# Optimization experiments

Hardware: AMD Instinct MI355X
Metric: run time of the kernel (lower is better)

Reference implementation:

```python
import jax, jax.numpy as jnp
import numpy as np
from jax import lax

B, C, KH, SH, K = 128, 256, 7, 31, 3
EPS = 1e-5
DN = ('NCHW', 'OIHW', 'NCHW')


def _bn(x, p):
    # p: (4, C) rows = gamma, beta, running_mean, running_var (eval-mode BN)
    g, b, m, v = p[0], p[1], p[2], p[3]
    inv = g / jnp.sqrt(v + EPS)
    return x * inv[None, :, None, None] + (b - m * inv)[None, :, None, None]


def _dwconv(x, w):
    # depthwise 3x3 VALID conv, w: (C,1,K,K)
    return lax.conv_general_dilated(x, w, (1, 1), 'VALID', dimension_numbers=DN,
                                    feature_group_count=x.shape[1])


def _pwconv(x, w, b):
    y = lax.conv_general_dilated(x, w, (1, 1), 'VALID', dimension_numbers=DN)
    return y + b[None, :, None, None]


def _relu6(x):
    return jnp.minimum(jax.nn.relu(x), 6.0)


def _branch(x, dw_w, bn1, pw_w, pw_b, bn2):
    # Conv(dw,3x3,no bias) -> BN -> ReLU6 -> Conv(1x1) -> BN
    return _bn(_pwconv(_relu6(_bn(_dwconv(x, dw_w), bn1)), pw_w, pw_b), bn2)


def _xcorr_depthwise(search, kernel):
    # per-sample, per-channel cross-correlation via groups = B*C conv trick
    b, c, hs, ws = search.shape
    hk, wk = kernel.shape[2], kernel.shape[3]
    x = search.reshape(1, b * c, hs, ws)
    k = kernel.reshape(b * c, 1, hk, wk)
    out = lax.conv_general_dilated(x, k, (1, 1), 'VALID', dimension_numbers=DN,
                                   feature_group_count=b * c)
    return out.reshape(b, c, out.shape[2], out.shape[3])


def _bn_params(key):
    k1, k2, k3, k4 = jax.random.split(key, 4)
    g = jax.random.uniform(k1, (C,), minval=0.5, maxval=1.5)
    b = jax.random.normal(k2, (C,)) * 0.1
    m = jax.random.normal(k3, (C,)) * 0.1
    v = jax.random.uniform(k4, (C,), minval=0.5, maxval=1.5)
    return jnp.stack([g, b, m, v]).astype(jnp.float32)


def setup_inputs() -> dict:
    key = jax.random.key(0)
    ks = jax.random.split(key, 10)
    dw_std = np.float32(np.sqrt(2.0 / (K * K * C)))   # torch init: normal(0, sqrt(2/n))
    pw_std = np.float32(np.sqrt(2.0 / C))
    return {
        'kernel': jax.random.normal(ks[0], (B, C, KH, KH), jnp.float32),
        'search': jax.random.normal(ks[1], (B, C, SH, SH), jnp.float32),
        'k_dw_w': jax.random.normal(ks[2], (C, 1, K, K), jnp.float32) * dw_std,
        'k_bn1': _bn_params(ks[3]),
        'k_pw_w': jax.random.normal(ks[4], (C, C, 1, 1), jnp.float32) * pw_std,
        'k_pw_b': jnp.zeros((C,), jnp.float32),
        'k_bn2': _bn_params(ks[5]),
        's_dw_w': jax.random.normal(ks[6], (C, 1, K, K), jnp.float32) * dw_std,
        's_bn1': _bn_params(ks[7]),
        's_pw_w': jax.random.normal(ks[8], (C, C, 1, 1), jnp.float32) * pw_std,
        's_pw_b': jnp.zeros((C,), jnp.float32),
        's_bn2': _bn_params(ks[9]),
    }


def reference(kernel, search, k_dw_w, k_bn1, k_pw_w, k_pw_b, k_bn2,
              s_dw_w, s_bn1, s_pw_w, s_pw_b, s_bn2):
    k = _branch(kernel, k_dw_w, k_bn1, k_pw_w, k_pw_b, k_bn2)   # (B,C,5,5)
    s = _branch(search, s_dw_w, s_bn1, s_pw_w, s_pw_b, s_bn2)   # (B,C,29,29)
    return _xcorr_depthwise(s, k)                                # (B,C,25,25)
```

## Files before the change

### kernel.cpp

```cpp
#include <hip/hip_runtime.h>

constexpr int B = 128, C = 256;
constexpr float EPS = 1e-5f;
constexpr int NSG = B * 841;
constexpr int NKG = B * 25;

typedef unsigned short u16;
typedef short short8 __attribute__((ext_vector_type(8)));
typedef u16 u16x8 __attribute__((ext_vector_type(8)));
typedef float f32x4 __attribute__((ext_vector_type(4)));

__device__ __forceinline__ u16 bf16_rne(float x) {
    unsigned u = __builtin_bit_cast(unsigned, x);
    return (u16)((u + 0x7FFFu + ((u >> 16) & 1u)) >> 16);
}
__device__ __forceinline__ float bf16_f(u16 h) {
    return __builtin_bit_cast(float, (unsigned)h << 16);
}

#define GLOAD16(g, l)                                                              \
    __builtin_amdgcn_global_load_lds(                                              \
        (const __attribute__((address_space(1))) unsigned int*)(g),                \
        (__attribute__((address_space(3))) unsigned int*)(l), 16, 0, 0)

__global__ __launch_bounds__(256)
void wprep3(const float* __restrict__ ws, const float* __restrict__ wk,
            u16* __restrict__ WtS, u16* __restrict__ WtK) {
    int i = blockIdx.x * 256 + threadIdx.x;
    int co = i >> 8, k = i & 255;
    int t = k >> 5, cg = co >> 4;
    int lane = ((k >> 3) & 3) * 16 + (co & 15);
    int e = k & 7;
    size_t o = ((size_t)(t * 16 + cg) * 64 + lane) * 8 + e;
    WtS[o] = bf16_rne(ws[i]);
    WtK[o] = bf16_rne(wk[i]);
}

template<int IN_H, int CG, int NSLICE>
__global__ __launch_bounds__(256)
void dw_pass8(const float* __restrict__ in, const float* __restrict__ dw_w,
              const float* __restrict__ bn1, u16* __restrict__ X3) {
    constexpr int OUT_H = IN_H - 2, ON = OUT_H * OUT_H, IHW = IN_H * IN_H;
    constexpr int NSTRIP = (OUT_H + 7) / 8;
    constexpr int NF4 = CG * IHW / 4;
    constexpr int SUBS = CG / 8;
    constexpr int NSP = B * ON;
    constexpr int PADC = CG + 2;
    __shared__ __align__(16) float S[2][NF4 * 4 + 16];
    __shared__ __align__(16) u16 xt[ON * PADC];

    const int tid = threadIdx.x;
    const int b = blockIdx.x;
    const int g0 = blockIdx.y * NSLICE;

    const bool active = tid < CG * OUT_H;
    int cl = 0, oh = 0;
    if (active) { cl = tid / OUT_H; oh = tid - cl * OUT_H; }

    auto issue_stage = [&](int buf, int g) {
        const float* src = in + ((size_t)b * C + g * CG) * IHW;
        #pragma unroll
        for (int ii = 0; ii < (NF4 + 255) / 256; ++ii) {
            int q = ii * 256 + tid;
            if (q < NF4) GLOAD16(src + q * 4, (char*)S[buf] + q * 16);
        }
    };

    issue_stage(0, g0);
    int cur = 0;

    for (int it = 0; it < NSLICE; ++it) {
        const int g = g0 + it;
        const int ci0 = g * CG;
        asm volatile("s_waitcnt vmcnt(0)" ::: "memory");
        __syncthreads();

        if (it + 1 < NSLICE) issue_stage(cur ^ 1, g0 + it + 1);

        u16 outv[NSTRIP][8];
        if (active) {
            const int ci = ci0 + cl;
            float wreg[9];
            #pragma unroll
            for (int q = 0; q < 9; ++q) wreg[q] = dw_w[ci * 9 + q];
            const float inv = bn1[ci] * rsqrtf(bn1[3 * C + ci] + EPS);
            const float shv = bn1[C + ci] - bn1[2 * C + ci] * inv;
            #pragma unroll
            for (int s = 0; s < NSTRIP; ++s) {
                float res[8] = {0.f, 0.f, 0.f, 0.f, 0.f, 0.f, 0.f, 0.f};
                #pragma unroll
                for (int dy = 0; dy < 3; ++dy) {
                    const float* r = S[cur] + cl * IHW + (oh + dy) * IN_H + s * 8;
                    float x[10];
                    #pragma unroll
                    for (int j = 0; j < 10; ++j) x[j] = r[j];
                    #pragma unroll
                    for (int o = 0; o < 8; ++o)
                        res[o] = fmaf(x[o], wreg[dy * 3],
                                  fmaf(x[o + 1], wreg[dy * 3 + 1],
                                   fmaf(x[o + 2], wreg[dy * 3 + 2], res[o])));
                }
                #pragma unroll
                for (int o = 0; o < 8; ++o) {
                    float y = res[o] * inv + shv;
                    y = fminf(fmaxf(y, 0.f), 6.f);
                    outv[s][o] = bf16_rne(y);
                }
            }
        }
        __syncthreads();

        if (active) {
            #pragma unroll
            for (int s = 0; s < NSTRIP; ++s) {
                const int ow0 = s * 8;
                #pragma unroll
                for (int o = 0; o < 8; ++o) {
                    if (ow0 + o < OUT_H) {
                        int n = oh * OUT_H + ow0 + o;
                        xt[n * PADC + cl] = outv[s][o];
                    }
                }
            }
        }
        __syncthreads();

        for (int q = tid; q < ON * SUBS; q += 256) {
            int sub = q / ON, n = q - sub * ON;
            const unsigned* w = (const unsigned*)xt + n * (PADC / 2) + sub * 4;
            uint4 v = {w[0], w[1], w[2], w[3]};
            u16* dst = X3 + ((size_t)(g * SUBS + sub) * NSP + (size_t)b * ON + n) * 8;
            *(uint4*)dst = v;
        }
        cur ^= 1;
    }
}

template<int IN_H, int CG>
__global__ __launch_bounds__(256)
void dw_pass7(const float* __restrict__ in, const float* __restrict__ dw_w,
              const float* __restrict__ bn1, u16* __restrict__ X3) {
    constexpr int OUT_H = IN_H - 2, ON = OUT_H * OUT_H, IHW = IN_H * IN_H;
    constexpr int NSTRIP = (OUT_H + 7) / 8;
    constexpr int NFLT = CG * IHW;
    constexpr int NF4 = NFLT / 4;
    constexpr int SUBS = CG / 8;
    constexpr int NSP = B * ON;
    constexpr int PADC = CG + 2;
    constexpr unsigned SM_IN = (NFLT + 16) * 4;
    constexpr unsigned SM_XT = (unsigned)ON * PADC * 2;
    constexpr unsigned SMSZ = SM_IN > SM_XT ? SM_IN : SM_XT;
    __shared__ __align__(16) char SMEM[SMSZ];
    float* S = (float*)SMEM;
    u16* xt = (u16*)SMEM;

    const int tid = threadIdx.x;
    const int b = blockIdx.x, g = blockIdx.y;
    const int ci0 = g * CG;
    const float* src = in + ((size_t)b * C + ci0) * IHW;

    for (int q = tid; q < NF4; q += 256)
        ((float4*)S)[q] = ((const float4*)src)[q];
    __syncthreads();

    const bool active = tid < CG * OUT_H;
    int cl = 0, oh = 0;
    if (active) { cl = tid / OUT_H; oh = tid - cl * OUT_H; }
    u16 outv[NSTRIP][8];
    if (active) {
        const int ci = ci0 + cl;
        float wreg[9];
        #pragma unroll
        for (int q = 0; q < 9; ++q) wreg[q] = dw_w[ci * 9 + q];
        const float inv = bn1[ci] * rsqrtf(bn1[3 * C + ci] + EPS);
        const float shv = bn1[C + ci] - bn1[2 * C + ci] * inv;
        #pragma unroll
        for (int s = 0; s < NSTRIP; ++s) {
            float res[8] = {0.f, 0.f, 0.f, 0.f, 0.f, 0.f, 0.f, 0.f};
            #pragma unroll
            for (int dy = 0; dy < 3; ++dy) {
                const float* r = S + cl * IHW + (oh + dy) * IN_H + s * 8;
                float x[10];
                #pragma unroll
                for (int j = 0; j < 10; ++j) x[j] = r[j];
                #pragma unroll
                for (int o = 0; o < 8; ++o)
                    res[o] = fmaf(x[o], wreg[dy * 3],
                              fmaf(x[o + 1], wreg[dy * 3 + 1],
                               fmaf(x[o + 2], wreg[dy * 3 + 2], res[o])));
            }
            #pragma unroll
            for (int o = 0; o < 8; ++o) {
                float y = res[o] * inv + shv;
                y = fminf(fmaxf(y, 0.f), 6.f);
                outv[s][o] = bf16_rne(y);
            }
        }
    }
    __syncthreads();

    if (active) {
        #pragma unroll
        for (int s = 0; s < NSTRIP; ++s) {
            const int ow0 = s * 8;
            #pragma unroll
            for (int o = 0; o < 8; ++o) {
                if (ow0 + o < OUT_H) {
                    int n = oh * OUT_H + ow0 + o;
                    xt[n * PADC + cl] = outv[s][o];
                }
            }
        }
    }
    __syncthreads();

    for (int q = tid; q < ON * SUBS; q += 256) {
        int sub = q / ON, n = q - sub * ON;
        const unsigned* w = (const unsigned*)xt + n * (PADC / 2) + sub * 4;
        uint4 v = {w[0], w[1], w[2], w[3]};
        u16* dst = X3 + ((size_t)(g * SUBS + sub) * NSP + (size_t)b * ON + n) * 8;
        *(uint4*)dst = v;
    }
}

template<int PQ>
__global__ __launch_bounds__(256)
void gemm7(const u16* __restrict__ X3, const u16* __restrict__ Wt,
           const float* __restrict__ pw_b, const float* __restrict__ bn2,
           u16* __restrict__ out) {
    constexpr int NSP = B * PQ;
    const int lane = threadIdx.x & 63, wave = threadIdx.x >> 6;
    const int lh = lane >> 4, ll = lane & 15;
    const int n0 = blockIdx.x * 64;

    f32x4 acc[4][4] = {};
    short8 bx0[4], aw0[4], bx1[4], aw1[4];

#define LOADX(t, bx)                                                            \
    {                                                                           \
        _Pragma("unroll")                                                       \
        for (int j = 0; j < 4; ++j) {                                           \
            size_t off = ((size_t)((t) * 4 + lh) * NSP + n0 + j * 16 + ll) * 8; \
            bx[j] = *(const short8*)(X3 + off);                                 \
        }                                                                       \
    }
#define LOADW(t, aw)                                                            \
    {                                                                           \
        _Pragma("unroll")                                                       \
        for (int i = 0; i < 4; ++i) {                                           \
            size_t off = ((size_t)((t) * 16 + wave * 4 + i) * 64 + lane) * 8;   \
            aw[i] = *(const short8*)(Wt + off);                                 \
        }                                                                       \
    }
#define MM(aw, bx)                                                              \
    {                                                                           \
        _Pragma("unroll")                                                       \
        for (int i = 0; i < 4; ++i) {                                           \
            _Pragma("unroll")                                                   \
            for (int j = 0; j < 4; ++j)                                         \
                acc[i][j] = __builtin_amdgcn_mfma_f32_16x16x32_bf16(aw[i], bx[j], acc[i][j], 0, 0, 0); \
        }                                                                       \
    }

    LOADX(0, bx0); LOADW(0, aw0);
    #pragma unroll
    for (int tt = 0; tt < 8; tt += 2) {
        if (tt + 1 < 8) { LOADX(tt + 1, bx1); LOADW(tt + 1, aw1); }
        MM(aw0, bx0);
        if (tt + 2 < 8) { LOADX(tt + 2, bx0); LOADW(tt + 2, aw0); }
        if (tt + 1 < 8) { MM(aw1, bx1); }
    }
#undef LOADX
#undef LOADW
#undef MM

    int bj[4], pj[4];
    #pragma unroll
    for (int j = 0; j < 4; ++j) {
        int nn = n0 + j * 16 + ll;
        bj[j] = nn / PQ; pj[j] = nn - bj[j] * PQ;
    }
    #pragma unroll
    for (int i = 0; i < 4; ++i) {
        #pragma unroll
        for (int r = 0; r < 4; ++r) {
            int co = wave * 64 + i * 16 + lh * 4 + r;
            float inv = bn2[co] * rsqrtf(bn2[3 * C + co] + EPS);
            float sh  = bn2[C + co] - bn2[2 * C + co] * inv + pw_b[co] * inv;
            #pragma unroll
            for (int j = 0; j < 4; ++j)
                out[((size_t)bj[j] * C + co) * PQ + pj[j]] = bf16_rne(acc[i][j][r] * inv + sh);
        }
    }
}

__global__ __launch_bounds__(256)
void xcorr3(const u16* __restrict__ s, const u16* __restrict__ k,
            float* __restrict__ out) {
    const int bc0 = blockIdx.x * 10;
    const int nbc = min(10, B * C - bc0);
    __shared__ float ss[10 * 841];
    __shared__ float ks[10 * 25];
    const int tid = threadIdx.x;
    for (int i = tid; i < nbc * 841; i += 256) ss[i] = bf16_f(s[(size_t)bc0 * 841 + i]);
    for (int i = tid; i < nbc * 25; i += 256) ks[i] = bf16_f(k[(size_t)bc0 * 25 + i]);
    __syncthreads();

    const int lb = tid / 25, lt = tid - lb * 25;
    if (lb >= nbc) return;
    const int ohg = lt / 5, owg = lt - ohg * 5;
    const float* sp = ss + lb * 841 + (ohg * 5) * 29 + owg * 5;
    float kk[25];
    #pragma unroll
    for (int q = 0; q < 25; ++q) kk[q] = ks[lb * 25 + q];

    float acc[5][5] = {};
    #pragma unroll
    for (int ir = 0; ir < 9; ++ir) {
        float row[9];
        #pragma unroll
        for (int j = 0; j < 9; ++j) row[j] = sp[ir * 29 + j];
        #pragma unroll
        for (int oi = 0; oi < 5; ++oi) {
            int ki = ir - oi;
            if (ki < 0 || ki > 4) continue;
            #pragma unroll
            for (int oj = 0; oj < 5; ++oj)
                #pragma unroll
                for (int kj = 0; kj < 5; ++kj)
                    acc[oi][oj] = fmaf(row[oj + kj], kk[ki * 5 + kj], acc[oi][oj]);
        }
    }
    float* op = out + (size_t)(bc0 + lb) * 625;
    #pragma unroll
    for (int oi = 0; oi < 5; ++oi)
        #pragma unroll
        for (int oj = 0; oj < 5; ++oj)
            op[(ohg * 5 + oi) * 25 + owg * 5 + oj] = acc[oi][oj];
}

template<int IN_H>
__global__ __launch_bounds__(256)
void branch_fallback(const float* __restrict__ in, const float* __restrict__ dw_w,
                     const float* __restrict__ bn1, const float* __restrict__ pw_w,
                     const float* __restrict__ pw_b, const float* __restrict__ bn2,
                     float* __restrict__ out) {
    constexpr int OUT_H = IN_H - 2;
    constexpr int P = OUT_H * OUT_H;
    const int n0  = blockIdx.x * 64;
    const int co0 = blockIdx.y * 64;
    const int tid = threadIdx.x;
    const int tx = tid & 15, ty = tid >> 4;
    __shared__ __align__(16) float Ws[16][64];
    __shared__ __align__(16) float Xs2[16][64];
    float acc[4][4] = {};
    for (int k0 = 0; k0 < C; k0 += 16) {
        #pragma unroll
        for (int e = 0; e < 4; e++) {
            int idx = e * 256 + tid;
            int m = idx & 63, kk = idx >> 6;
            Ws[kk][m] = pw_w[(co0 + m) * C + (k0 + kk)];
        }
        #pragma unroll
        for (int e = 0; e < 4; e++) {
            int idx = e * 256 + tid;
            int nn = idx & 63, kk = idx >> 6;
            int ci = k0 + kk;
            int n = n0 + nn;
            int b = n / P, p = n - b * P;
            int oh = p / OUT_H, ow = p - oh * OUT_H;
            const float* ip = in + (((size_t)b * C + ci) * IN_H + oh) * IN_H + ow;
            const float* wp = dw_w + ci * 9;
            float s = 0.f;
            #pragma unroll
            for (int dy = 0; dy < 3; dy++)
                #pragma unroll
                for (int dx = 0; dx < 3; dx++)
                    s = fmaf(ip[dy * IN_H + dx], wp[dy * 3 + dx], s);
            float inv = bn1[ci] * rsqrtf(bn1[3 * C + ci] + EPS);
            float y = s * inv + (bn1[C + ci] - bn1[2 * C + ci] * inv);
            Xs2[kk][nn] = fminf(fmaxf(y, 0.f), 6.f);
        }
        __syncthreads();
        #pragma unroll
        for (int kk = 0; kk < 16; kk++) {
            float4 av = *reinterpret_cast<const float4*>(&Ws[kk][ty * 4]);
            float4 bv = *reinterpret_cast<const float4*>(&Xs2[kk][tx * 4]);
            float a[4] = {av.x, av.y, av.z, av.w};
            float bb[4] = {bv.x, bv.y, bv.z, bv.w};
            #pragma unroll
            for (int i = 0; i < 4; i++)
                #pragma unroll
                for (int j = 0; j < 4; j++)
                    acc[i][j] = fmaf(a[i], bb[j], acc[i][j]);
        }
        __syncthreads();
    }
    #pragma unroll
    for (int i = 0; i < 4; i++) {
        int co = co0 + ty * 4 + i;
        float inv = bn2[co] * rsqrtf(bn2[3 * C + co] + EPS);
        float sh  = (bn2[C + co] - bn2[2 * C + co] * inv) + pw_b[co] * inv;
        int n = n0 + tx * 4;
        #pragma unroll
        for (int j = 0; j < 4; j++) {
            int nj = n + j;
            int bj2 = nj / P, pj2 = nj - bj2 * P;
            out[((size_t)bj2 * C + co) * P + pj2] = acc[i][j] * inv + sh;
        }
    }
}

__global__ __launch_bounds__(256)
void xcorr2f(const float* __restrict__ s, const float* __restrict__ k,
             float* __restrict__ out) {
    const int bc0 = blockIdx.x * 10;
    const int nbc = min(10, B * C - bc0);
    __shared__ float ss[10 * 841];
    __shared__ float ks[10 * 25];
    const int tid = threadIdx.x;
    for (int i = tid; i < nbc * 841; i += 256) ss[i] = s[(size_t)bc0 * 841 + i];
    for (int i = tid; i < nbc * 25; i += 256) ks[i] = k[(size_t)bc0 * 25 + i];
    __syncthreads();
    const int lb = tid / 25, lt = tid - lb * 25;
    if (lb >= nbc) return;
    const int ohg = lt / 5, owg = lt - ohg * 5;
    const float* sp = ss + lb * 841 + (ohg * 5) * 29 + owg * 5;
    float kk[25];
    #pragma unroll
    for (int q = 0; q < 25; ++q) kk[q] = ks[lb * 25 + q];
    float acc[5][5] = {};
    #pragma unroll
    for (int ir = 0; ir < 9; ++ir) {
        float row[9];
        #pragma unroll
        for (int j = 0; j < 9; ++j) row[j] = sp[ir * 29 + j];
        #pragma unroll
        for (int oi = 0; oi < 5; ++oi) {
            int ki = ir - oi;
            if (ki < 0 || ki > 4) continue;
            #pragma unroll
            for (int oj = 0; oj < 5; ++oj)
                #pragma unroll
                for (int kj = 0; kj < 5; ++kj)
                    acc[oi][oj] = fmaf(row[oj + kj], kk[ki * 5 + kj], acc[oi][oj]);
        }
    }
    float* op = out + (size_t)(bc0 + lb) * 625;
    #pragma unroll
    for (int oi = 0; oi < 5; ++oi)
        #pragma unroll
        for (int oj = 0; oj < 5; ++oj)
            op[(ohg * 5 + oi) * 25 + owg * 5 + oj] = acc[oi][oj];
}

extern "C" void kernel_launch(void* const* d_in, const int* in_sizes, int n_in,
                              void* d_out, int out_size, void* d_ws, size_t ws_size,
                              hipStream_t stream) {
    const float* kernel = (const float*)d_in[0];
    const float* search = (const float*)d_in[1];
    const float* k_dw_w = (const float*)d_in[2];
    const float* k_bn1  = (const float*)d_in[3];
    const float* k_pw_w = (const float*)d_in[4];
    const float* k_pw_b = (const float*)d_in[5];
    const float* k_bn2  = (const float*)d_in[6];
    const float* s_dw_w = (const float*)d_in[7];
    const float* s_bn1  = (const float*)d_in[8];
    const float* s_pw_w = (const float*)d_in[9];
    const float* s_pw_b = (const float*)d_in[10];
    const float* s_bn2  = (const float*)d_in[11];

    constexpr size_t SB_B  = (size_t)NSG * C * 2;
    constexpr size_t KB_B  = (size_t)NKG * C * 2;
    constexpr size_t X3S_B = (size_t)NSG * C * 2;
    constexpr size_t X3K_B = (size_t)NKG * C * 2;
    constexpr size_t W_B   = (size_t)C * C * 2;
    constexpr size_t NEED  = SB_B + KB_B + X3S_B + X3K_B + 2 * W_B;

    if (ws_size >= NEED) {
        char* base = (char*)d_ws;
        u16* Sb   = (u16*)base;   base += SB_B;
        u16* Kb   = (u16*)base;   base += KB_B;
        u16* X3s  = (u16*)base;   base += X3S_B;
        u16* X3k  = (u16*)base;   base += X3K_B;
        u16* WtS  = (u16*)base;   base += W_B;
        u16* WtK  = (u16*)base;

        wprep3<<<dim3(256), dim3(256), 0, stream>>>(s_pw_w, k_pw_w, WtS, WtK);
        dw_pass8<31, 8, 4><<<dim3(B, 8), dim3(256), 0, stream>>>(search, s_dw_w, s_bn1, X3s);
        dw_pass7<7, 32><<<dim3(B, 8), dim3(256), 0, stream>>>(kernel, k_dw_w, k_bn1, X3k);
        gemm7<841><<<dim3(NSG / 64), dim3(256), 0, stream>>>(X3s, WtS, s_pw_b, s_bn2, Sb);
        gemm7<25><<<dim3(NKG / 64), dim3(256), 0, stream>>>(X3k, WtK, k_pw_b, k_bn2, Kb);
        xcorr3<<<dim3((B * C + 9) / 10), dim3(256), 0, stream>>>(Sb, Kb, (float*)d_out);
    } else {
        float* s_buf = (float*)d_ws;
        float* k_buf = s_buf + (size_t)B * C * 29 * 29;
        branch_fallback<7><<<dim3(50, 4), dim3(256), 0, stream>>>(
            kernel, k_dw_w, k_bn1, k_pw_w, k_pw_b, k_bn2, k_buf);
        branch_fallback<31><<<dim3(1682, 4), dim3(256), 0, stream>>>(
            search, s_dw_w, s_bn1, s_pw_w, s_pw_b, s_bn2, s_buf);
        xcorr2f<<<dim3((B * C + 9) / 10), dim3(256), 0, stream>>>(s_buf, k_buf, (float*)d_out);
    }
}
```

Measured before the change: 142.6 us.

## Make search depthwise pass wave-local with per-wave LDS and no block barriers

The search-branch depthwise kernel changes from a 256-thread block that double-buffers four 8-channel slices with several __syncthreads per slice to 128-thread blocks in which each wave owns one 8-channel group. Each wave stages its group into a private LDS segment, computes the conv, BN and ReLU6 into registers, then reuses the same LDS as the transpose buffer, ordered only by waitcnt and scheduling barriers. The grid doubles and the intra-block pipelining goes away. This removes block-wide barrier stalls and raises the number of independent blocks, at the cost of no load/compute overlap within a wave and more registers per lane, since each lane handles several row tasks.

Result: slower. 155.3 us (+9.0%).

```diff
diff --git a/kernel.cpp b/kernel.cpp
--- a/kernel.cpp
+++ b/kernel.cpp
@@ -36,103 +36,109 @@
     WtK[o] = bf16_rne(wk[i]);
 }
 
-template<int IN_H, int CG, int NSLICE>
-__global__ __launch_bounds__(256)
-void dw_pass8(const float* __restrict__ in, const float* __restrict__ dw_w,
+template<int IN_H, int CG, int WPB>
+__global__ __launch_bounds__(WPB * 64)
+void dw_pass9(const float* __restrict__ in, const float* __restrict__ dw_w,
               const float* __restrict__ bn1, u16* __restrict__ X3) {
     constexpr int OUT_H = IN_H - 2, ON = OUT_H * OUT_H, IHW = IN_H * IN_H;
     constexpr int NSTRIP = (OUT_H + 7) / 8;
     constexpr int NF4 = CG * IHW / 4;
-    constexpr int SUBS = CG / 8;
     constexpr int NSP = B * ON;
     constexpr int PADC = CG + 2;
-    __shared__ __align__(16) float S[2][NF4 * 4 + 16];
-    __shared__ __align__(16) u16 xt[ON * PADC];
-
-    const int tid = threadIdx.x;
-    const int b = blockIdx.x;
-    const int g0 = blockIdx.y * NSLICE;
-
-    const bool active = tid < CG * OUT_H;
-    int cl = 0, oh = 0;
-    if (active) { cl = tid / OUT_H; oh = tid - cl * OUT_H; }
-
-    auto issue_stage = [&](int buf, int g) {
-        const float* src = in + ((size_t)b * C + g * CG) * IHW;
-        #pragma unroll
-        for (int ii = 0; ii < (NF4 + 255) / 256; ++ii) {
-            int q = ii * 256 + tid;
-            if (q < NF4) GLOAD16(src + q * 4, (char*)S[buf] + q * 16);
-        }
-    };
-
-    issue_stage(0, g0);
-    int cur = 0;
-
-    for (int it = 0; it < NSLICE; ++it) {
-        const int g = g0 + it;
-        const int ci0 = g * CG;
-        asm volatile("s_waitcnt vmcnt(0)" ::: "memory");
-        __syncthreads();
-
-        if (it + 1 < NSLICE) issue_stage(cur ^ 1, g0 + it + 1);
-
-        u16 outv[NSTRIP][8];
-        if (active) {
-            const int ci = ci0 + cl;
-            float wreg[9];
-            #pragma unroll
-            for (int q = 0; q < 9; ++q) wreg[q] = dw_w[ci * 9 + q];
-            const float inv = bn1[ci] * rsqrtf(bn1[3 * C + ci] + EPS);
-            const float shv = bn1[C + ci] - bn1[2 * C + ci] * inv;
-            #pragma unroll
-            for (int s = 0; s < NSTRIP; ++s) {
-                float res[8] = {0.f, 0.f, 0.f, 0.f, 0.f, 0.f, 0.f, 0.f};
-                #pragma unroll
-                for (int dy = 0; dy < 3; ++dy) {
-                    const float* r = S[cur] + cl * IHW + (oh + dy) * IN_H + s * 8;
-                    float x[10];
-                    #pragma unroll
-                    for (int j = 0; j < 10; ++j) x[j] = r[j];
-                    #pragma unroll
-                    for (int o = 0; o < 8; ++o)
-                        res[o] = fmaf(x[o], wreg[dy * 3],
-                                  fmaf(x[o + 1], wreg[dy * 3 + 1],
-                                   fmaf(x[o + 2], wreg[dy * 3 + 2], res[o])));
-                }
-                #pragma unroll
-                for (int o = 0; o < 8; ++o) {
-                    float y = res[o] * inv + shv;
-                    y = fminf(fmaxf(y, 0.f), 6.f);
-                    outv[s][o] = bf16_rne(y);
-                }
+    constexpr int RT = (CG * OUT_H + 63) / 64;
+    constexpr int SEG = ((NF4 * 16 + 63) / 64) * 64;
+    __shared__ __align__(16) char SMEM[WPB][SEG];
+
+    const int lane = threadIdx.x & 63, w = threadIdx.x >> 6;
+    const int b = blockIdx.x, g = blockIdx.y;
+    const int kc  = g * WPB + w;
+    const int ci0 = kc * CG;
+    char* S8 = SMEM[w];
+    const float* src = in + ((size_t)b * C + ci0) * IHW;
+
+    #pragma unroll
+    for (int r = 0; r < (NF4 + 63) / 64; ++r) {
+        int q = r * 64 + lane;
+        if (q < NF4) GLOAD16(src + q * 4, S8 + q * 16);
+    }
+    asm volatile("s_waitcnt vmcnt(0)" ::: "memory");
+    __builtin_amdgcn_sched_barrier(0);
+
+    const float* S = (const float*)S8;
+    u16* xt = (u16*)S8;
+
+    u16x8 ov[RT * NSTRIP];
+    bool actv[RT];
+    int clv[RT], ohv[RT];
+    #pragma unroll
+    for (int r = 0; r < RT; ++r) {
+        const int task = r * 64 + lane;
+        const bool act = task < CG * OUT_H;
+        actv[r] = act;
+        const int cl = act ? task / OUT_H : 0;
+        const int oh = act ? task - cl * OUT_H : 0;
+        clv[r] = cl; ohv[r] = oh;
+        const int ci = ci0 + cl;
+        float wreg[9];
+        #pragma unroll
+        for (int q = 0; q < 9; ++q) wreg[q] = dw_w[ci * 9 + q];
+        const float inv = bn1[ci] * rsqrtf(bn1[3 * C + ci] + EPS);
+        const float shv = bn1[C + ci] - bn1[2 * C + ci] * inv;
+        #pragma unroll
+        for (int s = 0; s < NSTRIP; ++s) {
+            float res[8] = {0.f, 0.f, 0.f, 0.f, 0.f, 0.f, 0.f, 0.f};
+            #pragma unroll
+            for (int dy = 0; dy < 3; ++dy) {
+                const float* rp = S + cl * IHW + (oh + dy) * IN_H + s * 8;
+                float x[10];
+                #pragma unroll
+                for (int j = 0; j < 10; ++j) x[j] = rp[j];
+                #pragma unroll
+                for (int o = 0; o < 8; ++o)
+                    res[o] = fmaf(x[o], wreg[dy * 3],
+                              fmaf(x[o + 1], wreg[dy * 3 + 1],
+                               fmaf(x[o + 2], wreg[dy * 3 + 2], res[o])));
             }
-        }
-        __syncthreads();
-
-        if (active) {
+            u16x8 pv;
+            #pragma unroll
+            for (int o = 0; o < 8; ++o) {
+                float y = res[o] * inv + shv;
+                y = fminf(fmaxf(y, 0.f), 6.f);
+                pv[o] = bf16_rne(y);
+            }
+            ov[r * NSTRIP + s] = pv;
+        }
+    }
+    asm volatile("s_waitcnt lgkmcnt(0)" ::: "memory");
+    __builtin_amdgcn_sched_barrier(0);
+
+    #pragma unroll
+    for (int r = 0; r < RT; ++r) {
+        if (actv[r]) {
             #pragma unroll
             for (int s = 0; s < NSTRIP; ++s) {
                 const int ow0 = s * 8;
                 #pragma unroll
                 for (int o = 0; o < 8; ++o) {
                     if (ow0 + o < OUT_H) {
-                        int n = oh * OUT_H + ow0 + o;
-                        xt[n * PADC + cl] = outv[s][o];
+                        int n = ohv[r] * OUT_H + ow0 + o;
+                        xt[n * PADC + clv[r]] = ov[r * NSTRIP + s][o];
                     }
                 }
             }
         }
-        __syncthreads();
-
-        for (int q = tid; q < ON * SUBS; q += 256) {
-            int sub = q / ON, n = q - sub * ON;
-            const unsigned* w = (const unsigned*)xt + n * (PADC / 2) + sub * 4;
-            uint4 v = {w[0], w[1], w[2], w[3]};
-            u16* dst = X3 + ((size_t)(g * SUBS + sub) * NSP + (size_t)b * ON + n) * 8;
-            *(uint4*)dst = v;
-        }
-        cur ^= 1;
+    }
+    asm volatile("s_waitcnt lgkmcnt(0)" ::: "memory");
+    __builtin_amdgcn_sched_barrier(0);
+
+    #pragma unroll
+    for (int r = 0; r < (ON + 63) / 64; ++r) {
+        int q = r * 64 + lane;
+        if (q < ON) {
+            const unsigned* wp = (const unsigned*)xt + q * (PADC / 2);
+            uint4 v = {wp[0], wp[1], wp[2], wp[3]};
+            *(uint4*)(X3 + ((size_t)kc * NSP + (size_t)b * ON + q) * 8) = v;
+        }
     }
 }
 
@@ -487,7 +493,7 @@
         u16* WtK  = (u16*)base;
 
         wprep3<<<dim3(256), dim3(256), 0, stream>>>(s_pw_w, k_pw_w, WtS, WtK);
-        dw_pass8<31, 8, 4><<<dim3(B, 8), dim3(256), 0, stream>>>(search, s_dw_w, s_bn1, X3s);
+        dw_pass9<31, 8, 2><<<dim3(B, 16), dim3(128), 0, stream>>>(search, s_dw_w, s_bn1, X3s);
         dw_pass7<7, 32><<<dim3(B, 8), dim3(256), 0, stream>>>(kernel, k_dw_w, k_bn1, X3k);
         gemm7<841><<<dim3(NSG / 64), dim3(256), 0, stream>>>(X3s, WtS, s_pw_b, s_bn2, Sb);
         gemm7<25><<<dim3(NKG / 64), dim3(256), 0, stream>>>(X3k, WtK, k_pw_b, k_bn2, Kb);
```
